# Kernel optimization log

Measured on AMD Instinct MI355X. Metric: run time of the kernel, lower is better.

Reference implementation:

```python
import jax, jax.numpy as jnp
import numpy as np

B, CDD, HIS, S, D, NH, FF, V, K = 8, 5, 50, 64, 768, 12, 3072, 30522, 8


def _ln(x):
    mu = x.mean(-1, keepdims=True)
    var = ((x - mu) ** 2).mean(-1, keepdims=True)
    return (x - mu) / jnp.sqrt(var + 1e-12)


def _transformer(x, mask, Wq, Wk, Wv, Wo, W1, W2):
    # x: [..., S, D]; mask: [..., S] (float, >0 means valid)
    lead = x.shape[:-2]
    s, d = x.shape[-2], x.shape[-1]
    dh = d // NH
    x2 = x.reshape(-1, s, d)
    m = mask.reshape(-1, s)
    split = lambda t: t.reshape(-1, s, NH, dh).transpose(0, 2, 1, 3)
    q, k, v = split(x2 @ Wq), split(x2 @ Wk), split(x2 @ Wv)
    logits = jnp.einsum('nhqd,nhkd->nhqk', q, k) / jnp.sqrt(jnp.float32(dh))
    logits = logits + jnp.where(m > 0, 0.0, -1e9)[:, None, None, :]
    a = jax.nn.softmax(logits, axis=-1)
    o = jnp.einsum('nhqk,nhkd->nhqd', a, v).transpose(0, 2, 1, 3).reshape(-1, s, d) @ Wo
    h = _ln(x2 + o)
    h = _ln(h + jax.nn.gelu(h @ W1) @ W2)
    h = h.reshape(*lead, s, d)
    return h, h[..., 0, :]


def _build_prefix(subword_index, mask):
    # subword_index: [B, n, S, 2] int; mask: [B, n, 1] float
    b, n = subword_index.shape[0], subword_index.shape[1]
    flat = subword_index[..., 0] * S + subword_index[..., 1]  # [B, n, S]
    dest = jnp.zeros((b * n, S * S), jnp.float32)
    dest = dest.at[jnp.arange(b * n)[:, None], flat.reshape(b * n, S)].set(1.0)
    dest = dest * mask.reshape(b * n, 1)
    prefix = dest.reshape(b, n, S, S)
    # granularity == 'avg' -> L1 normalize rows
    prefix = prefix / jnp.maximum(prefix.sum(-1, keepdims=True), 1e-12)
    return prefix


def setup_inputs() -> dict:
    key = jax.random.key(0)
    ks = jax.random.split(key, 24)
    w = lambda k, shp: jax.random.normal(k, shp, jnp.float32) * 0.02
    inp = {
        'cdd_subword_index': jax.random.randint(ks[0], (B, CDD, S, 2), 0, S, jnp.int32),
        'his_subword_index': jax.random.randint(ks[1], (B, HIS, S, 2), 0, S, jnp.int32),
        'cdd_encoded_index': jax.random.randint(ks[2], (B, CDD, S), 0, V, jnp.int32),
        'his_encoded_index': jax.random.randint(ks[3], (B, HIS, S), 0, V, jnp.int32),
        'cdd_mask': jnp.ones((B, CDD, 1), jnp.float32),
        'his_mask': jnp.ones((B, HIS, 1), jnp.float32),
        'cdd_attn_mask': jnp.ones((B, CDD, S), jnp.float32),
        'his_attn_mask': jnp.ones((B, HIS, S), jnp.float32),
        'emb': w(ks[4], (V, D)),
        'bert_Wq': w(ks[5], (D, D)), 'bert_Wk': w(ks[6], (D, D)),
        'bert_Wv': w(ks[7], (D, D)), 'bert_Wo': w(ks[8], (D, D)),
        'bert_W1': w(ks[9], (D, FF)), 'bert_W2': w(ks[10], (FF, D)),
        'encN_Wq': w(ks[11], (D, D)), 'encN_Wk': w(ks[12], (D, D)),
        'encN_Wv': w(ks[13], (D, D)), 'encN_Wo': w(ks[14], (D, D)),
        'encN_W1': w(ks[15], (D, FF)), 'encN_W2': w(ks[16], (FF, D)),
        'qU': w(ks[17], (D,)),
        'proj_W': w(ks[18], (D, D)), 'proj_b': jnp.zeros((D,), jnp.float32),
    }
    return inp


def reference(cdd_subword_index, his_subword_index, cdd_encoded_index, his_encoded_index,
              cdd_mask, his_mask, cdd_attn_mask, his_attn_mask, emb,
              bert_Wq, bert_Wk, bert_Wv, bert_Wo, bert_W1, bert_W2,
              encN_Wq, encN_Wk, encN_Wv, encN_Wo, encN_W1, encN_W2,
              qU, proj_W, proj_b):
    rt_d = jnp.sqrt(jnp.float32(D))
    # scatter-built one-hot subword->token prefix matrices
    cdd_prefix = _build_prefix(cdd_subword_index, cdd_mask)   # [B,C,S,S]
    his_prefix = _build_prefix(his_subword_index, his_mask)   # [B,H,S,S]
    # pooled attention masks: prefix @ mask
    cdd_attn = jnp.einsum('bcst,bct->bcs', cdd_prefix, cdd_attn_mask)
    his_attn = jnp.einsum('bnst,bnt->bns', his_prefix, his_attn_mask)
    # embedding lookup + subword->token pooling
    cdd_emb = jnp.einsum('bcst,bctd->bcsd', cdd_prefix, emb[cdd_encoded_index])
    his_emb = jnp.einsum('bnst,bntd->bnsd', his_prefix, emb[his_encoded_index])
    # candidate news: BERT encode, take CLS, project
    _, cdd_cls = _transformer(cdd_emb, cdd_attn, bert_Wq, bert_Wk, bert_Wv, bert_Wo, bert_W1, bert_W2)
    cdd_repr = jnp.tanh(cdd_cls @ proj_W + proj_b)            # [B,C,D]
    # history news encoder
    his_hidden, his_cls = _transformer(his_emb, his_attn, encN_Wq, encN_Wk, encN_Wv, encN_Wo, encN_W1, encN_W2)
    # user encoder: attention pooling over history news reprs
    wgt = jax.nn.softmax(jnp.einsum('bnd,d->bn', his_cls, qU) / rt_d, axis=-1)
    user0 = jnp.einsum('bn,bnd->bd', wgt, his_cls)            # [B,D]
    # matching reducer: top-k personalized terms per history news
    scores = jnp.einsum('bnsd,bd->bns', his_hidden, user0) / rt_d
    scores = jnp.where(his_attn > 0, scores, -1e9)
    _, kid = jax.lax.top_k(scores, K)                         # [B,H,K]
    ps_terms = jnp.take_along_axis(his_hidden, kid[..., None], axis=2).reshape(B, HIS * K, D)
    ps_mask = jnp.take_along_axis(his_attn, kid, axis=2).reshape(B, HIS * K)
    # user BERT over selected terms
    _, user_cls = _transformer(ps_terms, ps_mask, bert_Wq, bert_Wk, bert_Wv, bert_Wo, bert_W1, bert_W2)
    user_repr = jnp.tanh(user_cls @ proj_W + proj_b)          # [B,D]
    score = jnp.einsum('bcd,bd->bc', cdd_repr, user_repr) / rt_d
    prob = jax.nn.log_softmax(score, axis=1)
    return prob, kid
```

## Files before the change

### kernel.cpp

```cpp
#include <hip/hip_runtime.h>
#include <math.h>

#define DIM 768
#define NHEAD 12
#define DHEAD 64
#define FFDIM 3072

typedef _Float16 v8h __attribute__((ext_vector_type(8)));
typedef float v4f __attribute__((ext_vector_type(4)));

__device__ __forceinline__ float gelu_f(float x) {
    float x3 = x * x * x;
    return 0.5f * x * (1.0f + tanhf(0.7978845608028654f * (x + 0.044715f * x3)));
}

__device__ __forceinline__ void gl_lds16(const _Float16* g, _Float16* l) {
    __builtin_amdgcn_global_load_lds(
        (const __attribute__((address_space(1))) unsigned int*)(g),
        (__attribute__((address_space(3))) unsigned int*)(l),
        16, 0, 0);
}

struct GemmP {
    const _Float16* A1; const _Float16* A2;
    const _Float16* eB1[3]; const _Float16* eB2[3]; const _Float16* bB1[3];
    float* C[3];
    _Float16* G1; _Float16* G2;
    int bnd;
};

__global__ __launch_bounds__(256) void gemm_mfma(GemmP p, int M, int N, int K,
                                                 int epi, float cdiv, float gscale)
{
    __shared__ _Float16 sm[4][128 * 32];
    const int z = blockIdx.z;
    const int tid = threadIdx.x;
    const int w = tid >> 6, lane = tid & 63;
    const int lm = lane & 15, kg = lane >> 4;
    const int row0 = blockIdx.y << 7, col0 = blockIdx.x << 7;
    const int wm = (w >> 1) << 6, wn = (w & 1) << 6;
    const int rl = (w << 4) + (lane >> 2);
    const int cofs = (lane & 3) << 3;
    int nt; const _Float16 *B1p, *B2p;
    if (row0 < p.bnd) { nt = 3; B1p = p.eB1[z]; B2p = p.eB2[z]; }
    else             { nt = 1; B1p = p.bB1[z]; B2p = p.bB1[z]; }
    const _Float16* A1 = p.A1 + (size_t)row0 * K;
    const _Float16* A2 = p.A2 + (size_t)row0 * K;
    const _Float16* B1 = B1p + (size_t)col0 * K;
    const _Float16* B2 = B2p + (size_t)col0 * K;
    _Float16* sA1 = sm[0]; _Float16* sA2 = sm[1];
    _Float16* sB1 = sm[2]; _Float16* sB2 = sm[3];
    const int ldsLo = w * 512, ldsHi = (w + 4) * 512;

    v4f acc[4][4];
#pragma unroll
    for (int i = 0; i < 4; i++)
#pragma unroll
        for (int j = 0; j < 4; j++) acc[i][j] = (v4f){0.f, 0.f, 0.f, 0.f};

    for (int k0 = 0; k0 < K; k0 += 32) {
        __syncthreads();
        size_t glo = (size_t)rl * K + k0 + cofs;
        size_t ghi = glo + (size_t)64 * K;
        gl_lds16(A1 + glo, sA1 + ldsLo); gl_lds16(A1 + ghi, sA1 + ldsHi);
        gl_lds16(B1 + glo, sB1 + ldsLo); gl_lds16(B1 + ghi, sB1 + ldsHi);
        if (nt == 3) {
            gl_lds16(A2 + glo, sA2 + ldsLo); gl_lds16(A2 + ghi, sA2 + ldsHi);
            gl_lds16(B2 + glo, sB2 + ldsLo); gl_lds16(B2 + ghi, sB2 + ldsHi);
        }
        __syncthreads();
        v8h a1[4], b1f[4];
#pragma unroll
        for (int i = 0; i < 4; i++) {
            a1[i]  = *(const v8h*)(sA1 + (wm + (i << 4) + lm) * 32 + (kg << 3));
            b1f[i] = *(const v8h*)(sB1 + (wn + (i << 4) + lm) * 32 + (kg << 3));
        }
        if (nt == 3) {
            v8h a2[4], b2f[4];
#pragma unroll
            for (int i = 0; i < 4; i++) {
                a2[i]  = *(const v8h*)(sA2 + (wm + (i << 4) + lm) * 32 + (kg << 3));
                b2f[i] = *(const v8h*)(sB2 + (wn + (i << 4) + lm) * 32 + (kg << 3));
            }
#pragma unroll
            for (int i = 0; i < 4; i++)
#pragma unroll
                for (int j = 0; j < 4; j++) {
                    acc[i][j] = __builtin_amdgcn_mfma_f32_16x16x32_f16(a1[i], b1f[j], acc[i][j], 0, 0, 0);
                    acc[i][j] = __builtin_amdgcn_mfma_f32_16x16x32_f16(a1[i], b2f[j], acc[i][j], 0, 0, 0);
                    acc[i][j] = __builtin_amdgcn_mfma_f32_16x16x32_f16(a2[i], b1f[j], acc[i][j], 0, 0, 0);
                }
        } else {
#pragma unroll
            for (int i = 0; i < 4; i++)
#pragma unroll
                for (int j = 0; j < 4; j++)
                    acc[i][j] = __builtin_amdgcn_mfma_f32_16x16x32_f16(a1[i], b1f[j], acc[i][j], 0, 0, 0);
        }
    }
    float* C = p.C[z];
#pragma unroll
    for (int i = 0; i < 4; i++) {
        int rb = row0 + wm + (i << 4) + (kg << 2);
#pragma unroll
        for (int j = 0; j < 4; j++) {
            int cc = col0 + wn + (j << 4) + lm;
#pragma unroll
            for (int r = 0; r < 4; r++) {
                float c = acc[i][j][r] * cdiv;
                size_t idx = (size_t)(rb + r) * N + cc;
                if (epi == 0) {
                    C[idx] = c;
                } else {
                    float gv = gelu_f(c) * gscale;
                    _Float16 g1 = (_Float16)gv;
                    p.G1[idx] = g1;
                    p.G2[idx] = (_Float16)(gv - (float)g1);
                }
            }
        }
    }
}

struct WJobs {
    const float* src[12];
    _Float16* d1[12]; _Float16* d2[12];
    int K[12]; int N[12]; int start[12];
};
__global__ __launch_bounds__(256) void wsplit_tr(WJobs jb)
{
    __shared__ float sh[32 * 33];
    int bid = blockIdx.x;
    int ji = 0;
#pragma unroll
    for (int i = 1; i < 12; i++) if (bid >= jb.start[i]) ji = i;
    const float* src = jb.src[ji];
    _Float16* d1 = jb.d1[ji]; _Float16* d2 = jb.d2[ji];
    int K = jb.K[ji], N = jb.N[ji];
    int t = bid - jb.start[ji];
    int tilesN = N >> 5;
    int tk = t / tilesN, tn = t - tk * tilesN;
    int k0 = tk << 5, n0 = tn << 5;
    int c = threadIdx.x & 31, rr = threadIdx.x >> 5;
#pragma unroll
    for (int pph = 0; pph < 4; pph++) {
        int r = rr + (pph << 3);
        sh[c * 33 + r] = src[(size_t)(k0 + r) * N + n0 + c];
    }
    __syncthreads();
#pragma unroll
    for (int pph = 0; pph < 4; pph++) {
        int rn = rr + (pph << 3);
        float v = sh[rn * 33 + c] * 64.f;
        _Float16 b1 = (_Float16)v;
        size_t idx = (size_t)(n0 + rn) * K + k0 + c;
        d1[idx] = b1;
        if (d2) d2[idx] = (_Float16)(v - (float)b1);
    }
}

__global__ __launch_bounds__(256) void build_prefix2(const int* __restrict__ hisSub,
    const float* __restrict__ hisMask, const float* __restrict__ hisAmask,
    const int* __restrict__ cddSub, const float* __restrict__ cddMask,
    const float* __restrict__ cddAmask,
    float* __restrict__ P, float* __restrict__ hisA, float* __restrict__ cddA)
{
    __shared__ float pref[64 * 64];
    int g = blockIdx.x;
    const int* sub; const float* mask; const float* amask; float* aout; int li;
    if (g < 400) { sub = hisSub; mask = hisMask; amask = hisAmask; aout = hisA; li = g; }
    else         { sub = cddSub; mask = cddMask; amask = cddAmask; aout = cddA; li = g - 400; }
    int tid = threadIdx.x;
    for (int t = tid; t < 4096; t += 256) pref[t] = 0.f;
    __syncthreads();
    if (tid < 64) {
        int r = sub[((size_t)li * 64 + tid) * 2 + 0];
        int c = sub[((size_t)li * 64 + tid) * 2 + 1];
        pref[(r << 6) + c] = 1.0f;
    }
    __syncthreads();
    float m = mask[li];
    int lane = tid & 63, w = tid >> 6;
    for (int s = (w << 4); s < (w << 4) + 16; s++) {
        float v = pref[(s << 6) + lane] * m;
        float rs = v;
#pragma unroll
        for (int o = 32; o; o >>= 1) rs += __shfl_down(rs, o);
        rs = __shfl(rs, 0);
        float nv = v / fmaxf(rs, 1e-12f);
        P[(((size_t)g << 6) + s) * 64 + lane] = nv;
        float av = nv * amask[((size_t)li << 6) + lane];
#pragma unroll
        for (int o = 32; o; o >>= 1) av += __shfl_down(av, o);
        if (lane == 0) aout[((size_t)li << 6) + s] = av;
    }
}

__global__ __launch_bounds__(256) void emb_pool2(const float* __restrict__ P,
    const int* __restrict__ encHis, const int* __restrict__ encCdd,
    const float* __restrict__ emb, float* __restrict__ X,
    _Float16* __restrict__ s1, _Float16* __restrict__ s2, int gOffHis, int gMid)
{
    int gl = blockIdx.x >> 2, q = blockIdx.x & 3;
    int g; const int* enc;
    if (gl < gMid) { g = gOffHis + gl; enc = encHis + (size_t)g * 64; }
    else { int gc = gl - gMid; g = 400 + gc; enc = encCdd + (size_t)gc * 64; }
    int tid = threadIdx.x;
    __shared__ float pw[16][64];
    __shared__ int tk[64];
    if (tid < 64) tk[tid] = enc[tid];
    for (int u = tid; u < 1024; u += 256) {
        int si = u >> 6, t = u & 63;
        pw[si][t] = P[((size_t)g * 64 + q * 16 + si) * 64 + t];
    }
    __syncthreads();
    float acc[16][3];
#pragma unroll
    for (int si = 0; si < 16; si++) { acc[si][0] = 0.f; acc[si][1] = 0.f; acc[si][2] = 0.f; }
    for (int t = 0; t < 64; t++) {
        const float* er = emb + (size_t)tk[t] * DIM;
        float e0 = er[tid], e1 = er[tid + 256], e2 = er[tid + 512];
#pragma unroll
        for (int si = 0; si < 16; si++) {
            float w = pw[si][t];
            acc[si][0] = fmaf(w, e0, acc[si][0]);
            acc[si][1] = fmaf(w, e1, acc[si][1]);
            acc[si][2] = fmaf(w, e2, acc[si][2]);
        }
    }
#pragma unroll
    for (int si = 0; si < 16; si++) {
        size_t base = ((size_t)gl * 64 + q * 16 + si) * DIM;
#pragma unroll
        for (int cci = 0; cci < 3; cci++) {
            int cc = tid + (cci << 8);
            float v = acc[si][cci];
            X[base + cc] = v;
            float xs = v * 64.f;
            _Float16 a = (_Float16)xs;
            s1[base + cc] = a;
            s2[base + cc] = (_Float16)(xs - (float)a);
        }
    }
}

__global__ __launch_bounds__(256) void attn_fused64(const float* __restrict__ Q,
    const float* __restrict__ Km, const float* __restrict__ V,
    const float* __restrict__ maskHis, const float* __restrict__ maskCdd, int gMid,
    _Float16* __restrict__ o1, _Float16* __restrict__ o2)
{
    __shared__ float Ks[64 * 65];
    __shared__ float Vs[64 * 65];
    __shared__ float Qs[64 * 65];
    int h = blockIdx.x % NHEAD;
    int g = blockIdx.x / NHEAD;
    const float* mrow = (g < gMid) ? maskHis + (size_t)g * 64
                                   : maskCdd + (size_t)(g - gMid) * 64;
    int tid = threadIdx.x, lane = tid & 63, w = tid >> 6;
    {
        int r = tid >> 2, c0 = (tid & 3) << 4;
        const float* qp = Q  + ((size_t)g * 64 + r) * DIM + h * DHEAD + c0;
        const float* kp = Km + ((size_t)g * 64 + r) * DIM + h * DHEAD + c0;
        const float* vp = V  + ((size_t)g * 64 + r) * DIM + h * DHEAD + c0;
#pragma unroll
        for (int u = 0; u < 16; u += 4) {
            float4 qv = *(const float4*)(qp + u);
            float4 kv = *(const float4*)(kp + u);
            float4 vv = *(const float4*)(vp + u);
            int o = r * 65 + c0 + u;
            Qs[o+0]=qv.x; Qs[o+1]=qv.y; Qs[o+2]=qv.z; Qs[o+3]=qv.w;
            Ks[o+0]=kv.x; Ks[o+1]=kv.y; Ks[o+2]=kv.z; Ks[o+3]=kv.w;
            Vs[o+0]=vv.x; Vs[o+1]=vv.y; Vs[o+2]=vv.z; Vs[o+3]=vv.w;
        }
    }
    __syncthreads();
    float mk = mrow[lane] > 0.f ? 0.f : -1e9f;
    for (int il = 0; il < 16; il++) {
        int i = (w << 4) + il;
        float d = 0.f;
        for (int t = 0; t < 64; t++) d = fmaf(Qs[i * 65 + t], Ks[lane * 65 + t], d);
        float l = d * 0.125f + mk;
        float mx = l;
#pragma unroll
        for (int o = 32; o; o >>= 1) mx = fmaxf(mx, __shfl_xor(mx, o));
        float e = expf(l - mx);
        float s = e;
#pragma unroll
        for (int o = 32; o; o >>= 1) s += __shfl_xor(s, o);
        float p = e / s;
        float acc = 0.f;
        for (int j = 0; j < 64; j++) {
            float pj = __shfl(p, j);
            acc = fmaf(pj, Vs[j * 65 + lane], acc);
        }
        size_t ob = ((size_t)g * 64 + i) * DIM + h * DHEAD + lane;
        float os = acc * 64.f;
        _Float16 h1 = (_Float16)os;
        o1[ob] = h1;
        o2[ob] = (_Float16)(os - (float)h1);
    }
}

#define SSTR 449
__global__ __launch_bounds__(256) void attn_flash400(const float* __restrict__ Q,
    const float* __restrict__ Km, const float* __restrict__ V,
    const float* __restrict__ mask, _Float16* __restrict__ o1, _Float16* __restrict__ o2)
{
    __shared__ _Float16 Kt[64 * 64];
    __shared__ float Sc[16 * SSTR];
    int qt = blockIdx.x % 25;
    int h  = (blockIdx.x / 25) % NHEAD;
    int g  = blockIdx.x / (25 * NHEAD);
    int tid = threadIdx.x, w = tid >> 6, lane = tid & 63, lm = lane & 15, kg = lane >> 4;

    v8h aq0, aq1;
    {
        const float* qp = Q + ((size_t)(g * 400 + qt * 16 + lm)) * DIM + h * DHEAD;
#pragma unroll
        for (int u = 0; u < 8; u++) {
            aq0[u] = (_Float16)qp[kg * 8 + u];
            aq1[u] = (_Float16)qp[32 + kg * 8 + u];
        }
    }
    for (int jt = 0; jt < 7; jt++) {
        int j0 = jt * 64;
        __syncthreads();
        {
            int jr = tid >> 2, c0 = (tid & 3) << 4;
            int j = j0 + jr;
            _Float16* kd = Kt + jr * 64 + c0;
            if (j < 400) {
                const float* kp = Km + ((size_t)(g * 400 + j)) * DIM + h * DHEAD + c0;
#pragma unroll
                for (int u = 0; u < 16; u++) kd[u] = (_Float16)kp[u];
            } else {
#pragma unroll
                for (int u = 0; u < 16; u++) kd[u] = (_Float16)0.f;
            }
        }
        __syncthreads();
        v8h b0, b1;
#pragma unroll
        for (int u = 0; u < 8; u++) {
            b0[u] = Kt[(w * 16 + lm) * 64 + kg * 8 + u];
            b1[u] = Kt[(w * 16 + lm) * 64 + 32 + kg * 8 + u];
        }
        v4f c = {0.f, 0.f, 0.f, 0.f};
        c = __builtin_amdgcn_mfma_f32_16x16x32_f16(aq0, b0, c, 0, 0, 0);
        c = __builtin_amdgcn_mfma_f32_16x16x32_f16(aq1, b1, c, 0, 0, 0);
        int jj = j0 + w * 16 + lm;
        float mv = (jj < 400) ? (mask[g * 400 + jj] > 0.f ? 0.f : -1e9f) : -1e9f;
#pragma unroll
        for (int r = 0; r < 4; r++)
            Sc[(kg * 4 + r) * SSTR + jj] = c[r] * 0.125f + mv;
    }
    __syncthreads();
    for (int rr = 0; rr < 4; rr++) {
        int r = w * 4 + rr;
        float mx = -INFINITY;
#pragma unroll
        for (int c7 = 0; c7 < 7; c7++) mx = fmaxf(mx, Sc[r * SSTR + c7 * 64 + lane]);
#pragma unroll
        for (int o = 32; o; o >>= 1) mx = fmaxf(mx, __shfl_xor(mx, o));
        float s = 0.f;
        float ev[7];
#pragma unroll
        for (int c7 = 0; c7 < 7; c7++) { ev[c7] = expf(Sc[r * SSTR + c7 * 64 + lane] - mx); s += ev[c7]; }
#pragma unroll
        for (int o = 32; o; o >>= 1) s += __shfl_xor(s, o);
        float inv = 1.f / s;
#pragma unroll
        for (int c7 = 0; c7 < 7; c7++) Sc[r * SSTR + c7 * 64 + lane] = ev[c7] * inv;
    }
    __syncthreads();
    v4f o = {0.f, 0.f, 0.f, 0.f};
    for (int kc = 0; kc < 14; kc++) {
        v8h a, b;
#pragma unroll
        for (int u = 0; u < 8; u++) a[u] = (_Float16)Sc[lm * SSTR + kc * 32 + kg * 8 + u];
#pragma unroll
        for (int u = 0; u < 8; u++) {
            int j = kc * 32 + kg * 8 + u;
            b[u] = (j < 400) ? (_Float16)V[((size_t)(g * 400 + j)) * DIM + h * DHEAD + w * 16 + lm]
                             : (_Float16)0.f;
        }
        o = __builtin_amdgcn_mfma_f32_16x16x32_f16(a, b, o, 0, 0, 0);
    }
#pragma unroll
    for (int r = 0; r < 4; r++) {
        int qr = qt * 16 + kg * 4 + r;
        size_t ob = ((size_t)(g * 400 + qr)) * DIM + h * DHEAD + w * 16 + lm;
        float os = o[r] * 64.f;
        _Float16 h1 = (_Float16)os;
        o1[ob] = h1; o2[ob] = (_Float16)(os - (float)h1);
    }
}

__global__ __launch_bounds__(256) void add_ln2(const float* __restrict__ X,
    const float* __restrict__ Y, float* __restrict__ outA, float* __restrict__ outB,
    int bndRow, _Float16* __restrict__ S1, _Float16* __restrict__ S2, float ss,
    float* __restrict__ cls, int clsOffA, int clsOffB, int S)
{
    int r = blockIdx.x, tid = threadIdx.x;
    size_t base = (size_t)r * DIM;
    float v0 = X[base + tid] + Y[base + tid];
    float v1 = X[base + tid + 256] + Y[base + tid + 256];
    float v2 = X[base + tid + 512] + Y[base + tid + 512];
    __shared__ float red[256];
    red[tid] = v0 + v1 + v2; __syncthreads();
    for (int o = 128; o; o >>= 1) { if (tid < o) red[tid] += red[tid + o]; __syncthreads(); }
    float mu = red[0] * (1.f / 768.f);
    __syncthreads();
    float d0 = v0 - mu, d1 = v1 - mu, d2 = v2 - mu;
    red[tid] = d0 * d0 + d1 * d1 + d2 * d2; __syncthreads();
    for (int o = 128; o; o >>= 1) { if (tid < o) red[tid] += red[tid + o]; __syncthreads(); }
    float rstd = rsqrtf(red[0] * (1.f / 768.f) + 1e-12f);
    float o0 = d0 * rstd, o1 = d1 * rstd, o2 = d2 * rstd;
    float* Out = (r < bndRow) ? outA + base : outB + (size_t)(r - bndRow) * DIM;
    Out[tid] = o0; Out[tid + 256] = o1; Out[tid + 512] = o2;
    if (S1) {
        float x0 = o0 * ss, x1 = o1 * ss, x2 = o2 * ss;
        _Float16 a0 = (_Float16)x0, a1 = (_Float16)x1, a2 = (_Float16)x2;
        S1[base + tid] = a0;        S2[base + tid] = (_Float16)(x0 - (float)a0);
        S1[base + tid + 256] = a1;  S2[base + tid + 256] = (_Float16)(x1 - (float)a1);
        S1[base + tid + 512] = a2;  S2[base + tid + 512] = (_Float16)(x2 - (float)a2);
    }
    if (cls && (r % S) == 0) {
        int g = (r < bndRow) ? clsOffA + r / S : clsOffB + (r - bndRow) / S;
        float* cd = cls + (size_t)g * DIM;
        cd[tid] = o0; cd[tid + 256] = o1; cd[tid + 512] = o2;
    }
}

__global__ __launch_bounds__(256) void gemm_kernel(const float* __restrict__ A,
    const float* __restrict__ B, float* __restrict__ C,
    int M, int N, int Kd, int epi, const float* __restrict__ bias)
{
    __shared__ float As[16][64];
    __shared__ float Bs[16][64];
    int tid = threadIdx.x;
    int tx = tid & 15, ty = tid >> 4;
    int row0 = blockIdx.y << 6, col0 = blockIdx.x << 6;
    int ar = tid >> 2, ak = (tid & 3) << 2;
    int bc = tid & 63, bk0 = tid >> 6;
    const float* Ap = A + (size_t)(row0 + ar) * Kd + ak;
    const float* Bp = B + (size_t)bk0 * N + col0 + bc;
    bool aval = (row0 + ar) < M;
    float acc[4][4];
#pragma unroll
    for (int i = 0; i < 4; i++)
#pragma unroll
        for (int j = 0; j < 4; j++) acc[i][j] = 0.f;
    for (int k0 = 0; k0 < Kd; k0 += 16) {
        float4 a4 = make_float4(0.f, 0.f, 0.f, 0.f);
        if (aval) a4 = *(const float4*)(Ap + k0);
        As[ak + 0][ar] = a4.x; As[ak + 1][ar] = a4.y;
        As[ak + 2][ar] = a4.z; As[ak + 3][ar] = a4.w;
#pragma unroll
        for (int i = 0; i < 4; i++)
            Bs[bk0 + 4 * i][bc] = Bp[(size_t)(k0 + 4 * i) * N];
        __syncthreads();
#pragma unroll
        for (int kk = 0; kk < 16; kk++) {
            float4 av = *(const float4*)&As[kk][ty << 2];
            float4 bv = *(const float4*)&Bs[kk][tx << 2];
            float aa[4] = {av.x, av.y, av.z, av.w};
            float bb[4] = {bv.x, bv.y, bv.z, bv.w};
#pragma unroll
            for (int i = 0; i < 4; i++)
#pragma unroll
                for (int j = 0; j < 4; j++)
                    acc[i][j] = fmaf(aa[i], bb[j], acc[i][j]);
        }
        __syncthreads();
    }
#pragma unroll
    for (int i = 0; i < 4; i++) {
        int r = row0 + (ty << 2) + i;
        if (r >= M) continue;
        float v[4];
#pragma unroll
        for (int j = 0; j < 4; j++) {
            float x = acc[i][j];
            if (epi == 1) x = gelu_f(x);
            else if (epi == 2) x = tanhf(x + bias[col0 + (tx << 2) + j]);
            v[j] = x;
        }
        *(float4*)(C + (size_t)r * N + col0 + (tx << 2)) = make_float4(v[0], v[1], v[2], v[3]);
    }
}

__global__ __launch_bounds__(256) void user_pool_kernel(const float* __restrict__ cls,
    const float* __restrict__ qU, float* __restrict__ user0)
{
    int b = blockIdx.x, tid = threadIdx.x;
    __shared__ float red[256];
    __shared__ float wv[64];
    const float scale = 0.03608439182435161f;
    for (int n = 0; n < 50; n++) {
        const float* cr = cls + ((size_t)(b * 50 + n)) * DIM;
        float d = 0.f;
        for (int t = tid; t < DIM; t += 256) d = fmaf(cr[t], qU[t], d);
        red[tid] = d; __syncthreads();
        for (int o = 128; o; o >>= 1) { if (tid < o) red[tid] += red[tid + o]; __syncthreads(); }
        if (tid == 0) wv[n] = red[0] * scale;
        __syncthreads();
    }
    if (tid == 0) {
        float mx = -INFINITY;
        for (int n = 0; n < 50; n++) mx = fmaxf(mx, wv[n]);
        float s = 0.f;
        for (int n = 0; n < 50; n++) { float e = expf(wv[n] - mx); wv[n] = e; s += e; }
        float inv = 1.f / s;
        for (int n = 0; n < 50; n++) wv[n] *= inv;
    }
    __syncthreads();
    for (int d = tid; d < DIM; d += 256) {
        float a = 0.f;
        for (int n = 0; n < 50; n++) a = fmaf(wv[n], cls[((size_t)(b * 50 + n)) * DIM + d], a);
        user0[(size_t)b * DIM + d] = a;
    }
}

__global__ __launch_bounds__(256) void topk_kernel(const float* __restrict__ hid,
    const float* __restrict__ user0, const float* __restrict__ attn,
    float* __restrict__ kid_f, int* __restrict__ kid_i, float* __restrict__ ps_mask)
{
    int bn = blockIdx.x;
    int b = bn / 50;
    int tid = threadIdx.x, lane = tid & 63, w = tid >> 6;
    __shared__ float sc[64];
    const float* u = user0 + (size_t)b * DIM;
    const float scale = 0.03608439182435161f;
    for (int s = w; s < 64; s += 4) {
        const float* hr = hid + ((size_t)bn * 64 + s) * DIM;
        float d = 0.f;
        for (int t = lane; t < DIM; t += 64) d = fmaf(hr[t], u[t], d);
#pragma unroll
        for (int o = 32; o; o >>= 1) d += __shfl_down(d, o);
        if (lane == 0) {
            float a = attn[(size_t)bn * 64 + s];
            sc[s] = (a > 0.f) ? d * scale : -1e9f;
        }
    }
    __syncthreads();
    if (tid == 0) {
        unsigned long long used = 0ull;
        for (int k = 0; k < 8; k++) {
            float best = -INFINITY; int bi = 0;
            for (int s = 0; s < 64; s++) {
                if ((used >> s) & 1ull) continue;
                if (sc[s] > best) { best = sc[s]; bi = s; }
            }
            used |= (1ull << bi);
            kid_i[bn * 8 + k] = bi;
            kid_f[bn * 8 + k] = (float)bi;
            ps_mask[bn * 8 + k] = attn[(size_t)bn * 64 + bi];
        }
    }
}

__global__ void gather2(const float* __restrict__ hid, const int* __restrict__ kid_i,
    float* __restrict__ X, _Float16* __restrict__ s1, _Float16* __restrict__ s2)
{
    int r = blockIdx.x, tid = threadIdx.x;
    int s = kid_i[r];
    int bn = r >> 3;
    const float* src = hid + ((size_t)bn * 64 + s) * DIM;
    size_t base = (size_t)r * DIM;
#pragma unroll
    for (int cci = 0; cci < 3; cci++) {
        int cc = tid + (cci << 8);
        float v = src[cc];
        X[base + cc] = v;
        float xs = v * 64.f;
        _Float16 a = (_Float16)xs;
        s1[base + cc] = a;
        s2[base + cc] = (_Float16)(xs - (float)a);
    }
}

__global__ __launch_bounds__(256) void final_kernel(const float* __restrict__ cdd_repr,
    const float* __restrict__ user_repr, float* __restrict__ out)
{
    int b = blockIdx.x, tid = threadIdx.x;
    __shared__ float red[256];
    __shared__ float sc[5];
    const float scale = 0.03608439182435161f;
    for (int c = 0; c < 5; c++) {
        const float* cr = cdd_repr + ((size_t)(b * 5 + c)) * DIM;
        const float* ur = user_repr + (size_t)b * DIM;
        float d = 0.f;
        for (int t = tid; t < DIM; t += 256) d = fmaf(cr[t], ur[t], d);
        red[tid] = d; __syncthreads();
        for (int o = 128; o; o >>= 1) { if (tid < o) red[tid] += red[tid + o]; __syncthreads(); }
        if (tid == 0) sc[c] = red[0] * scale;
        __syncthreads();
    }
    if (tid == 0) {
        float mx = -INFINITY;
        for (int c = 0; c < 5; c++) mx = fmaxf(mx, sc[c]);
        float s = 0.f;
        for (int c = 0; c < 5; c++) s += expf(sc[c] - mx);
        float lse = logf(s) + mx;
        for (int c = 0; c < 5; c++) out[b * 5 + c] = sc[c] - lse;
    }
}

extern "C" void kernel_launch(void* const* d_in, const int* in_sizes, int n_in,
                              void* d_out, int out_size, void* d_ws, size_t ws_size,
                              hipStream_t stream)
{
    (void)in_sizes; (void)n_in; (void)out_size;
    const int*   cdd_sub   = (const int*)d_in[0];
    const int*   his_sub   = (const int*)d_in[1];
    const int*   cdd_enc   = (const int*)d_in[2];
    const int*   his_enc   = (const int*)d_in[3];
    const float* cdd_mask  = (const float*)d_in[4];
    const float* his_mask  = (const float*)d_in[5];
    const float* cdd_amask = (const float*)d_in[6];
    const float* his_amask = (const float*)d_in[7];
    const float* emb = (const float*)d_in[8];
    const float* bWsrc[6] = {(const float*)d_in[9],  (const float*)d_in[10], (const float*)d_in[11],
                             (const float*)d_in[12], (const float*)d_in[13], (const float*)d_in[14]};
    const float* eWsrc[6] = {(const float*)d_in[15], (const float*)d_in[16], (const float*)d_in[17],
                             (const float*)d_in[18], (const float*)d_in[19], (const float*)d_in[20]};
    const float* qU = (const float*)d_in[21];
    const float* pW = (const float*)d_in[22];
    const float* pb = (const float*)d_in[23];
    float* out = (float*)d_out;

    auto al256 = [](size_t b) { return (b + 255) & ~(size_t)255; };
    auto needBytes = [&](size_t RCx) -> size_t {
        size_t t = 0;
        t += 4 * al256(RCx * 768 * 4);
        t += 2 * al256(RCx * 768 * 2);
        t += al256(RCx * 3072 * 2);
        t += al256((size_t)440 * 4096 * 4);
        t += al256((size_t)400 * 64 * 768 * 4);
        t += al256((size_t)448 * 768 * 4);
        t += 8 * al256(131072);
        t += 3 * (4 * al256((size_t)589824 * 2) + 2 * al256((size_t)2359296 * 2));
        return t;
    };
    const int NSopts[9] = {400, 200, 134, 100, 66, 50, 34, 24, 10};
    int NS = 10;
    for (int i = 0; i < 9; i++) {
        size_t RCt = (size_t)NSopts[i] * 64 + 2560;
        if (needBytes(RCt) <= ws_size) { NS = NSopts[i]; break; }
    }
    const size_t RC = (size_t)NS * 64 + 2560;

    char* wsb = (char*)d_ws;
    size_t off = 0;
    auto allocB = [&](size_t bytes) { char* p = wsb + off; off += al256(bytes); return p; };
    float* R_X = (float*)allocB(RC * 768 * 4);
    float* R_Q = (float*)allocB(RC * 768 * 4);
    float* R_K = (float*)allocB(RC * 768 * 4);
    float* R_V = (float*)allocB(RC * 768 * 4);
    _Float16* s1h = (_Float16*)allocB(RC * 768 * 2);
    _Float16* s2h = (_Float16*)allocB(RC * 768 * 2);
    _Float16* g2h = (_Float16*)allocB(RC * 3072 * 2);
    float* Pa   = (float*)allocB((size_t)440 * 4096 * 4);
    float* hisH = (float*)allocB((size_t)400 * 64 * 768 * 4);
    float* cls  = (float*)allocB((size_t)448 * 768 * 4);
    float* userC = (float*)allocB(131072);
    float* hisA  = (float*)allocB(131072);
    float* cddA  = (float*)allocB(131072);
    float* cddR  = (float*)allocB(131072);
    float* userR = (float*)allocB(131072);
    float* user0 = (float*)allocB(131072);
    float* psM   = (float*)allocB(131072);
    int*   kidI  = (int*)allocB(131072);
    size_t wsz[6] = {589824, 589824, 589824, 589824, 2359296, 2359296};
    _Float16 *eB1s[6], *eB2s[6], *bB1s[6];
    for (int i = 0; i < 6; i++) eB1s[i] = (_Float16*)allocB(wsz[i] * 2);
    for (int i = 0; i < 6; i++) eB2s[i] = (_Float16*)allocB(wsz[i] * 2);
    for (int i = 0; i < 6; i++) bB1s[i] = (_Float16*)allocB(wsz[i] * 2);
    _Float16* g1h = (_Float16*)R_K;
    float* cddTrash = (float*)g2h;

    int wk[6] = {768, 768, 768, 768, 768, 3072};
    int wn[6] = {768, 768, 768, 768, 3072, 768};
    {
        WJobs jb{};
        int st = 0;
        for (int i = 0; i < 6; i++) {
            jb.src[i] = eWsrc[i]; jb.d1[i] = eB1s[i]; jb.d2[i] = eB2s[i];
            jb.K[i] = wk[i]; jb.N[i] = wn[i]; jb.start[i] = st;
            st += (wk[i] >> 5) * (wn[i] >> 5);
        }
        for (int i = 0; i < 6; i++) {
            jb.src[6 + i] = bWsrc[i]; jb.d1[6 + i] = bB1s[i]; jb.d2[6 + i] = nullptr;
            jb.K[6 + i] = wk[i]; jb.N[6 + i] = wn[i]; jb.start[6 + i] = st;
            st += (wk[i] >> 5) * (wn[i] >> 5);
        }
        wsplit_tr<<<st, 256, 0, stream>>>(jb);
    }

    build_prefix2<<<440, 256, 0, stream>>>(his_sub, his_mask, his_amask,
                                           cdd_sub, cdd_mask, cdd_amask, Pa, hisA, cddA);

    auto mkP = [&](int sl, int bnd) {
        GemmP g{};
        g.A1 = s1h; g.A2 = s2h;
        for (int z = 0; z < 3; z++) {
            g.eB1[z] = eB1s[sl]; g.eB2[z] = eB2s[sl]; g.bB1[z] = bB1s[sl];
        }
        g.bnd = bnd;
        return g;
    };

    auto tf = [&](int M, int bnd, int nseqTot, int gMid, const float* mHis,
                  float* outA, float* outB, float* clsArena, int clsOffA, int clsOffB,
                  int S, bool userAttn) {
        int MB = M >> 7;
        GemmP gq = mkP(0, bnd);
        for (int z = 0; z < 3; z++) { gq.eB1[z] = eB1s[z]; gq.eB2[z] = eB2s[z]; gq.bB1[z] = bB1s[z]; }
        gq.C[0] = R_Q; gq.C[1] = R_K; gq.C[2] = R_V;
        gemm_mfma<<<dim3(6, MB, 3), 256, 0, stream>>>(gq, M, 768, 768, 0, 1.f / 4096.f, 0.f);
        if (!userAttn) {
            attn_fused64<<<nseqTot * NHEAD, 256, 0, stream>>>(R_Q, R_K, R_V, mHis, cddA, gMid, s1h, s2h);
        } else {
            attn_flash400<<<8 * NHEAD * 25, 256, 0, stream>>>(R_Q, R_K, R_V, mHis, s1h, s2h);
        }
        GemmP go = mkP(3, bnd);
        go.C[0] = R_Q;
        gemm_mfma<<<dim3(6, MB, 1), 256, 0, stream>>>(go, M, 768, 768, 0, 1.f / 4096.f, 0.f);
        add_ln2<<<M, 256, 0, stream>>>(R_X, R_Q, R_X, R_X, M, s1h, s2h, 1.f, nullptr, 0, 0, 64);
        GemmP g1 = mkP(4, bnd);
        g1.G1 = g1h; g1.G2 = g2h;
        gemm_mfma<<<dim3(24, MB, 1), 256, 0, stream>>>(g1, M, 3072, 768, 1, 1.f / 64.f, 16.f);
        GemmP g2 = mkP(5, bnd);
        g2.A1 = g1h; g2.A2 = g2h; g2.C[0] = R_Q;
        gemm_mfma<<<dim3(6, MB, 1), 256, 0, stream>>>(g2, M, 768, 3072, 0, 1.f / 1024.f, 0.f);
        add_ln2<<<M, 256, 0, stream>>>(R_X, R_Q, outA, outB, bnd, nullptr, nullptr, 0.f,
                                       clsArena, clsOffA, clsOffB, S);
    };

    int done = 0;
    bool first = true;
    while (done < 400) {
        int ns = NS < (400 - done) ? NS : (400 - done);
        int hisRows = ns * 64;
        int M = hisRows + (first ? 2560 : 0);
        int nseqTot = ns + (first ? 40 : 0);
        emb_pool2<<<nseqTot * 4, 256, 0, stream>>>(Pa, his_enc, cdd_enc, emb, R_X, s1h, s2h, done, ns);
        tf(M, hisRows, nseqTot, ns, hisA + (size_t)done * 64,
           hisH + (size_t)done * 64 * DIM, cddTrash, cls, done, 400, 64, false);
        done += ns;
        first = false;
    }

    gemm_kernel<<<dim3(12, 1), 256, 0, stream>>>(cls + (size_t)400 * 768, pW, cddR, 40, 768, 768, 2, pb);

    user_pool_kernel<<<8, 256, 0, stream>>>(cls, qU, user0);
    topk_kernel<<<400, 256, 0, stream>>>(hisH, user0, hisA, out + 40, kidI, psM);
    gather2<<<3200, 256, 0, stream>>>(hisH, kidI, R_X, s1h, s2h);

    tf(3200, 0, 8, 0, psM, hisH, hisH, userC, 0, 0, 400, true);
    gemm_kernel<<<dim3(12, 1), 256, 0, stream>>>(userC, pW, userR, 8, 768, 768, 2, pb);

    final_kernel<<<8, 256, 0, stream>>>(cddR, userR, out);
}
```

Baseline: 3.236 ms.

## Double-buffer GEMM LDS tiles and remap workgroups per XCD for L2 locality

The MFMA GEMM now uses two LDS buffers, issuing the global-to-LDS loads for the next K slice before computing on the current one, with a single barrier per iteration instead of two. Workgroup IDs are also remapped so consecutive blocks on the same XCD share column groups (group size passed per launch), aiming to raise L2 reuse of weight tiles. The cost is doubled LDS use (64KB per block), which may reduce occupancy, plus some index arithmetic at the start of each block.

```diff
diff --git a/kernel.cpp b/kernel.cpp
--- a/kernel.cpp
+++ b/kernel.cpp
@@ -30,14 +30,27 @@
 };
 
 __global__ __launch_bounds__(256) void gemm_mfma(GemmP p, int M, int N, int K,
-                                                 int epi, float cdiv, float gscale)
-{
-    __shared__ _Float16 sm[4][128 * 32];
-    const int z = blockIdx.z;
+                                                 int epi, float cdiv, float gscale, int nbg)
+{
+    __shared__ _Float16 sm[2][4][128 * 32];
     const int tid = threadIdx.x;
     const int w = tid >> 6, lane = tid & 63;
     const int lm = lane & 15, kg = lane >> 4;
-    const int row0 = blockIdx.y << 7, col0 = blockIdx.x << 7;
+
+    const int nb = (int)gridDim.x, mb = (int)gridDim.y;
+    const int nwg = nb * mb * (int)gridDim.z;
+    int lid = (int)blockIdx.x + nb * ((int)blockIdx.y + mb * (int)blockIdx.z);
+    int qd = nwg >> 3, rm = nwg & 7;
+    int xcd = lid & 7, pos = lid >> 3;
+    int wid = (xcd < rm ? xcd * (qd + 1) : rm * (qd + 1) + (xcd - rm) * qd) + pos;
+    int gsz = (nbg > 0 && (nb % nbg) == 0) ? nbg : 1;
+    int ngrp = nb / gsz;
+    int bxi = wid % gsz; int tt = wid / gsz;
+    int by = tt % mb; tt /= mb;
+    int bxg = tt % ngrp;
+    int z = tt / ngrp;
+    const int row0 = by << 7, col0 = (bxg * gsz + bxi) << 7;
+
     const int wm = (w >> 1) << 6, wn = (w & 1) << 6;
     const int rl = (w << 4) + (lane >> 2);
     const int cofs = (lane & 3) << 3;
@@ -48,9 +61,8 @@
     const _Float16* A2 = p.A2 + (size_t)row0 * K;
     const _Float16* B1 = B1p + (size_t)col0 * K;
     const _Float16* B2 = B2p + (size_t)col0 * K;
-    _Float16* sA1 = sm[0]; _Float16* sA2 = sm[1];
-    _Float16* sB1 = sm[2]; _Float16* sB2 = sm[3];
     const int ldsLo = w * 512, ldsHi = (w + 4) * 512;
+    const size_t gbase = (size_t)rl * K + cofs;
 
     v4f acc[4][4];
 #pragma unroll
@@ -58,45 +70,54 @@
 #pragma unroll
         for (int j = 0; j < 4; j++) acc[i][j] = (v4f){0.f, 0.f, 0.f, 0.f};
 
-    for (int k0 = 0; k0 < K; k0 += 32) {
-        __syncthreads();
-        size_t glo = (size_t)rl * K + k0 + cofs;
+    auto stage = [&](int d, int k0) {
+        size_t glo = gbase + k0;
         size_t ghi = glo + (size_t)64 * K;
-        gl_lds16(A1 + glo, sA1 + ldsLo); gl_lds16(A1 + ghi, sA1 + ldsHi);
-        gl_lds16(B1 + glo, sB1 + ldsLo); gl_lds16(B1 + ghi, sB1 + ldsHi);
+        gl_lds16(A1 + glo, sm[d][0] + ldsLo); gl_lds16(A1 + ghi, sm[d][0] + ldsHi);
+        gl_lds16(B1 + glo, sm[d][2] + ldsLo); gl_lds16(B1 + ghi, sm[d][2] + ldsHi);
         if (nt == 3) {
-            gl_lds16(A2 + glo, sA2 + ldsLo); gl_lds16(A2 + ghi, sA2 + ldsHi);
-            gl_lds16(B2 + glo, sB2 + ldsLo); gl_lds16(B2 + ghi, sB2 + ldsHi);
-        }
-        __syncthreads();
+            gl_lds16(A2 + glo, sm[d][1] + ldsLo); gl_lds16(A2 + ghi, sm[d][1] + ldsHi);
+            gl_lds16(B2 + glo, sm[d][3] + ldsLo); gl_lds16(B2 + ghi, sm[d][3] + ldsHi);
+        }
+    };
+
+    const int nk = K >> 5;
+    stage(0, 0);
+    __syncthreads();
+    for (int i = 0; i < nk; i++) {
+        int cur = i & 1;
+        if (i + 1 < nk) stage(cur ^ 1, (i + 1) << 5);
+        const _Float16* sA1 = sm[cur][0]; const _Float16* sA2 = sm[cur][1];
+        const _Float16* sB1 = sm[cur][2]; const _Float16* sB2 = sm[cur][3];
         v8h a1[4], b1f[4];
 #pragma unroll
-        for (int i = 0; i < 4; i++) {
-            a1[i]  = *(const v8h*)(sA1 + (wm + (i << 4) + lm) * 32 + (kg << 3));
-            b1f[i] = *(const v8h*)(sB1 + (wn + (i << 4) + lm) * 32 + (kg << 3));
+        for (int i2 = 0; i2 < 4; i2++) {
+            a1[i2]  = *(const v8h*)(sA1 + (wm + (i2 << 4) + lm) * 32 + (kg << 3));
+            b1f[i2] = *(const v8h*)(sB1 + (wn + (i2 << 4) + lm) * 32 + (kg << 3));
         }
         if (nt == 3) {
             v8h a2[4], b2f[4];
 #pragma unroll
-            for (int i = 0; i < 4; i++) {
-                a2[i]  = *(const v8h*)(sA2 + (wm + (i << 4) + lm) * 32 + (kg << 3));
-                b2f[i] = *(const v8h*)(sB2 + (wn + (i << 4) + lm) * 32 + (kg << 3));
+            for (int i2 = 0; i2 < 4; i2++) {
+                a2[i2]  = *(const v8h*)(sA2 + (wm + (i2 << 4) + lm) * 32 + (kg << 3));
+                b2f[i2] = *(const v8h*)(sB2 + (wn + (i2 << 4) + lm) * 32 + (kg << 3));
             }
 #pragma unroll
-            for (int i = 0; i < 4; i++)
+            for (int i2 = 0; i2 < 4; i2++)
 #pragma unroll
                 for (int j = 0; j < 4; j++) {
-                    acc[i][j] = __builtin_amdgcn_mfma_f32_16x16x32_f16(a1[i], b1f[j], acc[i][j], 0, 0, 0);
-                    acc[i][j] = __builtin_amdgcn_mfma_f32_16x16x32_f16(a1[i], b2f[j], acc[i][j], 0, 0, 0);
-                    acc[i][j] = __builtin_amdgcn_mfma_f32_16x16x32_f16(a2[i], b1f[j], acc[i][j], 0, 0, 0);
+                    acc[i2][j] = __builtin_amdgcn_mfma_f32_16x16x32_f16(a1[i2], b1f[j], acc[i2][j], 0, 0, 0);
+                    acc[i2][j] = __builtin_amdgcn_mfma_f32_16x16x32_f16(a1[i2], b2f[j], acc[i2][j], 0, 0, 0);
+                    acc[i2][j] = __builtin_amdgcn_mfma_f32_16x16x32_f16(a2[i2], b1f[j], acc[i2][j], 0, 0, 0);
                 }
         } else {
 #pragma unroll
-            for (int i = 0; i < 4; i++)
+            for (int i2 = 0; i2 < 4; i2++)
 #pragma unroll
                 for (int j = 0; j < 4; j++)
-                    acc[i][j] = __builtin_amdgcn_mfma_f32_16x16x32_f16(a1[i], b1f[j], acc[i][j], 0, 0, 0);
-        }
+                    acc[i2][j] = __builtin_amdgcn_mfma_f32_16x16x32_f16(a1[i2], b1f[j], acc[i2][j], 0, 0, 0);
+        }
+        __syncthreads();
     }
     float* C = p.C[z];
 #pragma unroll
@@ -718,7 +739,7 @@
         GemmP gq = mkP(0, bnd);
         for (int z = 0; z < 3; z++) { gq.eB1[z] = eB1s[z]; gq.eB2[z] = eB2s[z]; gq.bB1[z] = bB1s[z]; }
         gq.C[0] = R_Q; gq.C[1] = R_K; gq.C[2] = R_V;
-        gemm_mfma<<<dim3(6, MB, 3), 256, 0, stream>>>(gq, M, 768, 768, 0, 1.f / 4096.f, 0.f);
+        gemm_mfma<<<dim3(6, MB, 3), 256, 0, stream>>>(gq, M, 768, 768, 0, 1.f / 4096.f, 0.f, 6);
         if (!userAttn) {
             attn_fused64<<<nseqTot * NHEAD, 256, 0, stream>>>(R_Q, R_K, R_V, mHis, cddA, gMid, s1h, s2h);
         } else {
@@ -726,14 +747,14 @@
         }
         GemmP go = mkP(3, bnd);
         go.C[0] = R_Q;
-        gemm_mfma<<<dim3(6, MB, 1), 256, 0, stream>>>(go, M, 768, 768, 0, 1.f / 4096.f, 0.f);
+        gemm_mfma<<<dim3(6, MB, 1), 256, 0, stream>>>(go, M, 768, 768, 0, 1.f / 4096.f, 0.f, 6);
         add_ln2<<<M, 256, 0, stream>>>(R_X, R_Q, R_X, R_X, M, s1h, s2h, 1.f, nullptr, 0, 0, 64);
         GemmP g1 = mkP(4, bnd);
         g1.G1 = g1h; g1.G2 = g2h;
-        gemm_mfma<<<dim3(24, MB, 1), 256, 0, stream>>>(g1, M, 3072, 768, 1, 1.f / 64.f, 16.f);
+        gemm_mfma<<<dim3(24, MB, 1), 256, 0, stream>>>(g1, M, 3072, 768, 1, 1.f / 64.f, 16.f, 6);
         GemmP g2 = mkP(5, bnd);
         g2.A1 = g1h; g2.A2 = g2h; g2.C[0] = R_Q;
-        gemm_mfma<<<dim3(6, MB, 1), 256, 0, stream>>>(g2, M, 768, 3072, 0, 1.f / 1024.f, 0.f);
+        gemm_mfma<<<dim3(6, MB, 1), 256, 0, stream>>>(g2, M, 768, 3072, 0, 1.f / 1024.f, 0.f, 2);
         add_ln2<<<M, 256, 0, stream>>>(R_X, R_Q, outA, outB, bnd, nullptr, nullptr, 0.f,
                                        clsArena, clsOffA, clsOffB, S);
     };
```

Result: faster. 3.160 ms (-2.3%).
